# Performance work log

Measured on AMD Instinct MI355X. Metric: run time of the kernel, lower is better.

## Reference

```python
import jax, jax.numpy as jnp
import numpy as np

WIDTH = 8  # fixed-point fractional bits (init arg Width)


def quantizer(x, width=WIDTH):
    # Fixed-point quantization to `width` fractional bits, clipped to [-1, 1].
    scale = jnp.asarray(2.0 ** width, x.dtype)
    return jnp.clip(jnp.round(x * scale) / scale, -1.0, 1.0)


def setup_inputs() -> dict:
    key = jax.random.key(0)
    k1, k2, k3 = jax.random.split(key, 3)
    N, H, W, C = 32, 56, 56, 128
    KH, KW, F = 3, 3, 256
    OH, OW = H - KH + 1, W - KW + 1  # valid padding, stride 1
    x = jax.random.normal(k1, (N, H, W, C), dtype=jnp.float32) * 0.5
    kernels = jax.random.normal(k2, (KH, KW, C, F), dtype=jnp.float32) * 0.01
    bias = jax.random.normal(k3, (OH, OW, F), dtype=jnp.float32) * 0.01
    return {"x": x, "kernels": kernels, "bias": bias}


def reference(x, kernels, bias):
    # Method == 'Fixed': quantize input and kernels, valid conv, quantize output,
    # then per-position bias add + ReLU.
    xq = quantizer(x)
    wq = quantizer(kernels)
    out = jax.lax.conv_general_dilated(
        xq, wq,
        window_strides=(1, 1),
        padding="VALID",
        dimension_numbers=("NHWC", "HWIO", "NHWC"),
    )
    out = quantizer(out)
    return jax.nn.relu(out + bias[None, :, :, :])
```

## Files before the change

kernel.cpp:

```cpp
#include <hip/hip_runtime.h>
#include <hip/hip_bf16.h>
#include <stdint.h>
#include <stddef.h>


typedef float  f32x4  __attribute__((ext_vector_type(4)));
typedef short  bf16x8 __attribute__((ext_vector_type(8)));

#define N_IMG 32
#define H_IN 56
#define W_IN 56
#define C_IN 128
#define F_OUT 256
#define OHW 54
#define M_TOTAL (N_IMG * OHW * OHW)
#define BM 128
#define BN 128
#define BK 64

__device__ __forceinline__ unsigned short quant_to_bf16(float x) {
    float a = rintf(x * 256.0f);
    a = fminf(fmaxf(a, -256.0f), 256.0f);
    float q = a * 0.00390625f;
    union { float f; unsigned int u; } cv; cv.f = q;
    return (unsigned short)(cv.u >> 16);
}

__device__ __forceinline__ void async_copy16(const unsigned short* g, unsigned short* l) {
    __builtin_amdgcn_global_load_lds(
        (const __attribute__((address_space(1))) unsigned int*)g,
        (__attribute__((address_space(3))) unsigned int*)l, 16, 0, 0);
}

__global__ __launch_bounds__(256) void quant_x_kernel(
        const float* __restrict__ x, unsigned short* __restrict__ xq) {
    int i = (blockIdx.x * 256 + threadIdx.x) * 4;
    float4 v = *reinterpret_cast<const float4*>(x + i);
    ushort4 o;
    o.x = quant_to_bf16(v.x);
    o.y = quant_to_bf16(v.y);
    o.z = quant_to_bf16(v.z);
    o.w = quant_to_bf16(v.w);
    *reinterpret_cast<ushort4*>(xq + i) = o;
}

__global__ __launch_bounds__(256) void quant_w_kernel(
        const float* __restrict__ w, unsigned short* __restrict__ wp) {
    int idx = blockIdx.x * 256 + threadIdx.x;
    int c  = idx & 127;
    int f  = (idx >> 7) & 255;
    int kk = idx >> 15;
    float v = w[(kk * C_IN + c) * F_OUT + f];
    wp[idx] = quant_to_bf16(v);
}

__global__ __launch_bounds__(256) void conv_kernel(
        const unsigned short* __restrict__ xq,
        const unsigned short* __restrict__ wp,
        const float* __restrict__ bias,
        float* __restrict__ out)
{
    __shared__ __attribute__((aligned(16))) unsigned short Alds[BM * BK];
    __shared__ __attribute__((aligned(16))) unsigned short Blds[BN * BK];

    const int tid  = threadIdx.x;
    const int wave = tid >> 6;
    const int lane = tid & 63;
    const int bid  = blockIdx.x;
    const int mb   = bid >> 1;
    const int nb   = bid & 1;
    const int m0   = mb * BM;
    const int wr   = wave >> 1;
    const int wc   = wave & 1;

    const int c16  = tid & 7;
    const int row0 = tid >> 3;
    const int sw   = c16 ^ (row0 & 7);

    const unsigned short* a_base[4];
#pragma unroll
    for (int r = 0; r < 4; ++r) {
        int m = m0 + row0 + 32 * r;
        int n_img = m / (OHW * OHW);
        int rem   = m % (OHW * OHW);
        int oh = rem / OHW, ow = rem % OHW;
        a_base[r] = xq + (size_t)((n_img * H_IN + oh) * W_IN + ow) * C_IN + sw * 8;
    }
    const unsigned short* b_base[4];
#pragma unroll
    for (int r = 0; r < 4; ++r) {
        int f = nb * BN + row0 + 32 * r;
        b_base[r] = wp + (size_t)f * C_IN + sw * 8;
    }
    unsigned short* a_dst[4];
    unsigned short* b_dst[4];
#pragma unroll
    for (int r = 0; r < 4; ++r) {
        int cb = r * 256 + (tid & ~63);
        a_dst[r] = Alds + cb * 8;
        b_dst[r] = Blds + cb * 8;
    }

    const int mr = lane & 15;
    const int lq = lane >> 4;
    const int ls = lane & 7;

    f32x4 acc[4][4];
#pragma unroll
    for (int i = 0; i < 4; ++i)
#pragma unroll
        for (int j = 0; j < 4; ++j) acc[i][j] = (f32x4)(0.0f);

    for (int kk = 0; kk < 9; ++kk) {
        const int kh = kk / 3, kw = kk - 3 * kh;
        const int atap = (kh * W_IN + kw) * C_IN;
        const int btap = kk * (F_OUT * C_IN);
#pragma unroll
        for (int half = 0; half < 2; ++half) {
            const int aoff = atap + half * 64;
            const int boff = btap + half * 64;

            __syncthreads();
#pragma unroll
            for (int r = 0; r < 4; ++r)
                async_copy16(a_base[r] + aoff, a_dst[r]);
#pragma unroll
            for (int r = 0; r < 4; ++r)
                async_copy16(b_base[r] + boff, b_dst[r]);
            __syncthreads();

#pragma unroll
            for (int ks = 0; ks < 2; ++ks) {
                bf16x8 af[4], bfr[4];
#pragma unroll
                for (int mi = 0; mi < 4; ++mi)
                    af[mi] = *reinterpret_cast<const bf16x8*>(
                        Alds + (wr * 64 + mi * 16 + mr) * BK + (((ks * 4 + lq) ^ ls) * 8));
#pragma unroll
                for (int ni = 0; ni < 4; ++ni)
                    bfr[ni] = *reinterpret_cast<const bf16x8*>(
                        Blds + (wc * 64 + ni * 16 + mr) * BK + (((ks * 4 + lq) ^ ls) * 8));
#pragma unroll
                for (int mi = 0; mi < 4; ++mi)
#pragma unroll
                    for (int ni = 0; ni < 4; ++ni)
                        acc[mi][ni] = __builtin_amdgcn_mfma_f32_16x16x32_bf16(
                            af[mi], bfr[ni], acc[mi][ni], 0, 0, 0);
            }
        }
    }

    const int fcol0 = nb * BN + wc * 64 + mr;
#pragma unroll
    for (int mi = 0; mi < 4; ++mi) {
#pragma unroll
        for (int r = 0; r < 4; ++r) {
            const int m = m0 + wr * 64 + mi * 16 + lq * 4 + r;
            const float* brow = bias + (size_t)(m % (OHW * OHW)) * F_OUT;
            float* orow = out + (size_t)m * F_OUT;
#pragma unroll
            for (int ni = 0; ni < 4; ++ni) {
                float v = acc[mi][ni][r];
                float t = rintf(v * 256.0f);
                t = fminf(fmaxf(t, -256.0f), 256.0f);
                float o = t * 0.00390625f + brow[fcol0 + ni * 16];
                orow[fcol0 + ni * 16] = fmaxf(o, 0.0f);
            }
        }
    }
}

extern "C" void kernel_launch(void* const* d_in, const int* in_sizes, int n_in,
                              void* d_out, int out_size, void* d_ws, size_t ws_size,
                              hipStream_t stream) {
    (void)in_sizes; (void)n_in; (void)out_size;
    const float* x    = (const float*)d_in[0];
    const float* w    = (const float*)d_in[1];
    const float* bias = (const float*)d_in[2];
    float* out        = (float*)d_out;

    const size_t x_elems = (size_t)N_IMG * H_IN * W_IN * C_IN;
    const size_t w_elems = (size_t)9 * F_OUT * C_IN;
    const size_t xq_bytes = x_elems * sizeof(unsigned short);
    const size_t need = xq_bytes + w_elems * sizeof(unsigned short);
    if (ws_size < need) return;

    unsigned short* xq = (unsigned short*)d_ws;
    unsigned short* wp = (unsigned short*)((char*)d_ws + xq_bytes);

    quant_x_kernel<<<(int)(x_elems / (256 * 4)), 256, 0, stream>>>(x, xq);
    quant_w_kernel<<<(int)(w_elems / 256), 256, 0, stream>>>(w, wp);
    conv_kernel<<<(M_TOTAL / BM) * 2, 256, 0, stream>>>(xq, wp, bias, out);
}
```

Baseline: 92.80 us.

## Triple-buffer LDS pipeline with full-width N tile and 512-thread blocks

```diff
diff --git a/kernel.cpp b/kernel.cpp
--- a/kernel.cpp
+++ b/kernel.cpp
@@ -15,8 +15,13 @@
 #define OHW 54
 #define M_TOTAL (N_IMG * OHW * OHW)
 #define BM 128
-#define BN 128
+#define BN 256
 #define BK 64
+#define NTILES 18
+#define A_BUF_SHORTS (BM * BK)
+#define B_BUF_SHORTS (BN * BK)
+#define A_BUF_BYTES (A_BUF_SHORTS * 2)
+#define B_BUF_BYTES (B_BUF_SHORTS * 2)
 
 __device__ __forceinline__ unsigned short quant_to_bf16(float x) {
     float a = rintf(x * 256.0f);
@@ -30,6 +35,16 @@
     __builtin_amdgcn_global_load_lds(
         (const __attribute__((address_space(1))) unsigned int*)g,
         (__attribute__((address_space(3))) unsigned int*)l, 16, 0, 0);
+}
+
+__device__ __forceinline__ unsigned lds_off(const void* p) {
+    return (unsigned)(uintptr_t)(__attribute__((address_space(3))) const void*)p;
+}
+
+__device__ __forceinline__ bf16x8 lds_read_b128(unsigned addr) {
+    bf16x8 r;
+    asm volatile("ds_read_b128 %0, %1" : "=v"(r) : "v"(addr));
+    return r;
 }
 
 __global__ __launch_bounds__(256) void quant_x_kernel(
@@ -50,60 +65,65 @@
     int c  = idx & 127;
     int f  = (idx >> 7) & 255;
     int kk = idx >> 15;
-    float v = w[(kk * C_IN + c) * F_OUT + f];
-    wp[idx] = quant_to_bf16(v);
-}
-
-__global__ __launch_bounds__(256) void conv_kernel(
+    wp[idx] = quant_to_bf16(w[(kk * C_IN + c) * F_OUT + f]);
+}
+
+__global__ __launch_bounds__(512, 2) void conv_kernel(
         const unsigned short* __restrict__ xq,
         const unsigned short* __restrict__ wp,
         const float* __restrict__ bias,
         float* __restrict__ out)
 {
-    __shared__ __attribute__((aligned(16))) unsigned short Alds[BM * BK];
-    __shared__ __attribute__((aligned(16))) unsigned short Blds[BN * BK];
+    __shared__ __attribute__((aligned(16))) unsigned short Alds[3][A_BUF_SHORTS];
+    __shared__ __attribute__((aligned(16))) unsigned short Blds[3][B_BUF_SHORTS];
 
     const int tid  = threadIdx.x;
+    const int lane = tid & 63;
     const int wave = tid >> 6;
-    const int lane = tid & 63;
-    const int bid  = blockIdx.x;
-    const int mb   = bid >> 1;
-    const int nb   = bid & 1;
-    const int m0   = mb * BM;
-    const int wr   = wave >> 1;
-    const int wc   = wave & 1;
-
+    const int wr   = wave >> 2;
+    const int wc   = wave & 3;
+    const int m0   = blockIdx.x * BM;
+
+    const int rowt = tid >> 3;
     const int c16  = tid & 7;
-    const int row0 = tid >> 3;
-    const int sw   = c16 ^ (row0 & 7);
-
-    const unsigned short* a_base[4];
-#pragma unroll
-    for (int r = 0; r < 4; ++r) {
-        int m = m0 + row0 + 32 * r;
+    const int sw   = c16 ^ (rowt & 7);
+    const int dstc = tid & ~63;
+
+    const unsigned short* a_src[2];
+#pragma unroll
+    for (int r = 0; r < 2; ++r) {
+        int m = m0 + 64 * r + rowt;
         int n_img = m / (OHW * OHW);
         int rem   = m % (OHW * OHW);
         int oh = rem / OHW, ow = rem % OHW;
-        a_base[r] = xq + (size_t)((n_img * H_IN + oh) * W_IN + ow) * C_IN + sw * 8;
+        a_src[r] = xq + (size_t)((n_img * H_IN + oh) * W_IN + ow) * C_IN + sw * 8;
     }
-    const unsigned short* b_base[4];
-#pragma unroll
-    for (int r = 0; r < 4; ++r) {
-        int f = nb * BN + row0 + 32 * r;
-        b_base[r] = wp + (size_t)f * C_IN + sw * 8;
-    }
-    unsigned short* a_dst[4];
-    unsigned short* b_dst[4];
-#pragma unroll
-    for (int r = 0; r < 4; ++r) {
-        int cb = r * 256 + (tid & ~63);
-        a_dst[r] = Alds + cb * 8;
-        b_dst[r] = Blds + cb * 8;
-    }
+    const unsigned short* b_src[4];
+#pragma unroll
+    for (int r = 0; r < 4; ++r)
+        b_src[r] = wp + (size_t)(64 * r + rowt) * C_IN + sw * 8;
 
     const int mr = lane & 15;
     const int lq = lane >> 4;
-    const int ls = lane & 7;
+    unsigned a_rd[4][2], b_rd[4][2];
+    const unsigned Abase = lds_off(&Alds[0][0]);
+    const unsigned Bbase = lds_off(&Blds[0][0]);
+#pragma unroll
+    for (int mi = 0; mi < 4; ++mi)
+#pragma unroll
+        for (int ks = 0; ks < 2; ++ks) {
+            int row = wr * 64 + mi * 16 + mr;
+            int ch  = (ks * 4 + lq) ^ (mr & 7);
+            a_rd[mi][ks] = Abase + row * (BK * 2) + ch * 16;
+        }
+#pragma unroll
+    for (int ni = 0; ni < 4; ++ni)
+#pragma unroll
+        for (int ks = 0; ks < 2; ++ks) {
+            int row = wc * 64 + ni * 16 + mr;
+            int ch  = (ks * 4 + lq) ^ (mr & 7);
+            b_rd[ni][ks] = Bbase + row * (BK * 2) + ch * 16;
+        }
 
     f32x4 acc[4][4];
 #pragma unroll
@@ -111,56 +131,109 @@
 #pragma unroll
         for (int j = 0; j < 4; ++j) acc[i][j] = (f32x4)(0.0f);
 
-    for (int kk = 0; kk < 9; ++kk) {
-        const int kh = kk / 3, kw = kk - 3 * kh;
-        const int atap = (kh * W_IN + kw) * C_IN;
-        const int btap = kk * (F_OUT * C_IN);
-#pragma unroll
-        for (int half = 0; half < 2; ++half) {
-            const int aoff = atap + half * 64;
-            const int boff = btap + half * 64;
-
-            __syncthreads();
-#pragma unroll
-            for (int r = 0; r < 4; ++r)
-                async_copy16(a_base[r] + aoff, a_dst[r]);
-#pragma unroll
-            for (int r = 0; r < 4; ++r)
-                async_copy16(b_base[r] + boff, b_dst[r]);
-            __syncthreads();
-
-#pragma unroll
-            for (int ks = 0; ks < 2; ++ks) {
-                bf16x8 af[4], bfr[4];
-#pragma unroll
-                for (int mi = 0; mi < 4; ++mi)
-                    af[mi] = *reinterpret_cast<const bf16x8*>(
-                        Alds + (wr * 64 + mi * 16 + mr) * BK + (((ks * 4 + lq) ^ ls) * 8));
-#pragma unroll
-                for (int ni = 0; ni < 4; ++ni)
-                    bfr[ni] = *reinterpret_cast<const bf16x8*>(
-                        Blds + (wc * 64 + ni * 16 + mr) * BK + (((ks * 4 + lq) ^ ls) * 8));
-#pragma unroll
-                for (int mi = 0; mi < 4; ++mi)
-#pragma unroll
-                    for (int ni = 0; ni < 4; ++ni)
-                        acc[mi][ni] = __builtin_amdgcn_mfma_f32_16x16x32_bf16(
-                            af[mi], bfr[ni], acc[mi][ni], 0, 0, 0);
-            }
-        }
+    auto stage_p0 = [&](int tt, int bi) {
+        int kk = tt >> 1, half = tt & 1;
+        int kh = (kk * 43) >> 7, kw = kk - 3 * kh;
+        int aoff = (kh * W_IN + kw) * C_IN + half * 64;
+        int boff = kk * (F_OUT * C_IN) + half * 64;
+        async_copy16(a_src[0] + aoff, &Alds[bi][dstc * 8]);
+        async_copy16(a_src[1] + aoff, &Alds[bi][(512 + dstc) * 8]);
+        async_copy16(b_src[0] + boff, &Blds[bi][dstc * 8]);
+    };
+    auto stage_p1 = [&](int tt, int bi) {
+        int kk = tt >> 1, half = tt & 1;
+        int boff = kk * (F_OUT * C_IN) + half * 64;
+        async_copy16(b_src[1] + boff, &Blds[bi][(512 + dstc) * 8]);
+        async_copy16(b_src[2] + boff, &Blds[bi][(1024 + dstc) * 8]);
+        async_copy16(b_src[3] + boff, &Blds[bi][(1536 + dstc) * 8]);
+    };
+
+    auto do_tile = [&](int cur, int stage_tt, bool dostage, int endmode) {
+        const unsigned ca = (unsigned)cur * A_BUF_BYTES;
+        const unsigned cb = (unsigned)cur * B_BUF_BYTES;
+        int bi = cur + 2; if (bi >= 3) bi -= 3;
+
+        bf16x8 af[4][2], bq[2][2];
+#pragma unroll
+        for (int mi = 0; mi < 4; ++mi)
+#pragma unroll
+            for (int ks = 0; ks < 2; ++ks)
+                af[mi][ks] = lds_read_b128(a_rd[mi][ks] + ca);
+#pragma unroll
+        for (int ni = 0; ni < 2; ++ni)
+#pragma unroll
+            for (int ks = 0; ks < 2; ++ks)
+                bq[ni][ks] = lds_read_b128(b_rd[ni][ks] + cb);
+        if (dostage) stage_p0(stage_tt, bi);
+        asm volatile("" ::: "memory");
+        __builtin_amdgcn_s_barrier();
+        asm volatile("s_waitcnt lgkmcnt(0)" ::: "memory");
+        __builtin_amdgcn_sched_barrier(0);
+        __builtin_amdgcn_s_setprio(1);
+#pragma unroll
+        for (int mi = 0; mi < 4; ++mi)
+#pragma unroll
+            for (int ni = 0; ni < 2; ++ni)
+#pragma unroll
+                for (int ks = 0; ks < 2; ++ks)
+                    acc[mi][ni] = __builtin_amdgcn_mfma_f32_16x16x32_bf16(
+                        af[mi][ks], bq[ni][ks], acc[mi][ni], 0, 0, 0);
+        __builtin_amdgcn_s_setprio(0);
+        asm volatile("" ::: "memory");
+        __builtin_amdgcn_s_barrier();
+
+#pragma unroll
+        for (int ni = 0; ni < 2; ++ni)
+#pragma unroll
+            for (int ks = 0; ks < 2; ++ks)
+                bq[ni][ks] = lds_read_b128(b_rd[ni + 2][ks] + cb);
+        if (dostage) stage_p1(stage_tt, bi);
+        asm volatile("" ::: "memory");
+        __builtin_amdgcn_s_barrier();
+        asm volatile("s_waitcnt lgkmcnt(0)" ::: "memory");
+        __builtin_amdgcn_sched_barrier(0);
+        __builtin_amdgcn_s_setprio(1);
+#pragma unroll
+        for (int mi = 0; mi < 4; ++mi)
+#pragma unroll
+            for (int ni = 0; ni < 2; ++ni)
+#pragma unroll
+                for (int ks = 0; ks < 2; ++ks)
+                    acc[mi][ni + 2] = __builtin_amdgcn_mfma_f32_16x16x32_bf16(
+                        af[mi][ks], bq[ni][ks], acc[mi][ni + 2], 0, 0, 0);
+        __builtin_amdgcn_s_setprio(0);
+        if (endmode == 0)      asm volatile("s_waitcnt vmcnt(6)" ::: "memory");
+        else if (endmode == 1) asm volatile("s_waitcnt vmcnt(0)" ::: "memory");
+        if (endmode <= 1) {
+            asm volatile("" ::: "memory");
+            __builtin_amdgcn_s_barrier();
+        }
+    };
+
+    stage_p0(0, 0); stage_p1(0, 0);
+    stage_p0(1, 1); stage_p1(1, 1);
+    asm volatile("s_waitcnt vmcnt(6)" ::: "memory");
+    __builtin_amdgcn_s_barrier();
+
+#pragma unroll 1
+    for (int t = 0; t < 16; ++t) {
+        int cur = t - (t / 3) * 3;
+        do_tile(cur, t + 2, true, 0);
     }
-
-    const int fcol0 = nb * BN + wc * 64 + mr;
+    do_tile(1, 0, false, 1);
+    do_tile(2, 0, false, 2);
+
+    const int fcol0 = wc * 64 + mr;
 #pragma unroll
     for (int mi = 0; mi < 4; ++mi) {
 #pragma unroll
-        for (int r = 0; r < 4; ++r) {
-            const int m = m0 + wr * 64 + mi * 16 + lq * 4 + r;
+        for (int rr = 0; rr < 4; ++rr) {
+            const int m = m0 + wr * 64 + mi * 16 + lq * 4 + rr;
             const float* brow = bias + (size_t)(m % (OHW * OHW)) * F_OUT;
             float* orow = out + (size_t)m * F_OUT;
 #pragma unroll
             for (int ni = 0; ni < 4; ++ni) {
-                float v = acc[mi][ni][r];
+                float v = acc[mi][ni][rr];
                 float t = rintf(v * 256.0f);
                 t = fminf(fmaxf(t, -256.0f), 256.0f);
                 float o = t * 0.00390625f + brow[fcol0 + ni * 16];
@@ -190,5 +263,5 @@
 
     quant_x_kernel<<<(int)(x_elems / (256 * 4)), 256, 0, stream>>>(x, xq);
     quant_w_kernel<<<(int)(w_elems / 256), 256, 0, stream>>>(w, wp);
-    conv_kernel<<<(M_TOTAL / BM) * 2, 256, 0, stream>>>(xq, wp, bias, out);
-}
+    conv_kernel<<<M_TOTAL / BM, 512, 0, stream>>>(xq, wp, bias, out);
+}
```

New measurement: 94.98 us. 2.3% more time.

## Double-buffer LDS tiles so async global loads overlap MFMA compute

Applied to the files above, without the earlier changes.

```diff
diff --git a/kernel.cpp b/kernel.cpp
--- a/kernel.cpp
+++ b/kernel.cpp
@@ -50,18 +50,17 @@
     int c  = idx & 127;
     int f  = (idx >> 7) & 255;
     int kk = idx >> 15;
-    float v = w[(kk * C_IN + c) * F_OUT + f];
-    wp[idx] = quant_to_bf16(v);
+    wp[idx] = quant_to_bf16(w[(kk * C_IN + c) * F_OUT + f]);
 }
 
-__global__ __launch_bounds__(256) void conv_kernel(
+__global__ __launch_bounds__(256, 2) void conv_kernel(
         const unsigned short* __restrict__ xq,
         const unsigned short* __restrict__ wp,
         const float* __restrict__ bias,
         float* __restrict__ out)
 {
-    __shared__ __attribute__((aligned(16))) unsigned short Alds[BM * BK];
-    __shared__ __attribute__((aligned(16))) unsigned short Blds[BN * BK];
+    __shared__ __attribute__((aligned(16))) unsigned short Alds[2][BM * BK];
+    __shared__ __attribute__((aligned(16))) unsigned short Blds[2][BN * BK];
 
     const int tid  = threadIdx.x;
     const int wave = tid >> 6;
@@ -73,9 +72,9 @@
     const int wr   = wave >> 1;
     const int wc   = wave & 1;
 
-    const int c16  = tid & 7;
     const int row0 = tid >> 3;
-    const int sw   = c16 ^ (row0 & 7);
+    const int sw   = (tid & 7) ^ (row0 & 7);
+    const int dstc = (tid & ~63) * 8;
 
     const unsigned short* a_base[4];
 #pragma unroll
@@ -88,22 +87,24 @@
     }
     const unsigned short* b_base[4];
 #pragma unroll
-    for (int r = 0; r < 4; ++r) {
-        int f = nb * BN + row0 + 32 * r;
-        b_base[r] = wp + (size_t)f * C_IN + sw * 8;
-    }
-    unsigned short* a_dst[4];
-    unsigned short* b_dst[4];
+    for (int r = 0; r < 4; ++r)
+        b_base[r] = wp + (size_t)(nb * BN + row0 + 32 * r) * C_IN + sw * 8;
+
+    auto stage = [&](int t, unsigned short* Ab, unsigned short* Bb) {
+        int kk = t >> 1, hf = t & 1;
+        int kh = (kk * 43) >> 7, kw = kk - 3 * kh;
+        int aoff = (kh * W_IN + kw) * C_IN + hf * 64;
+        int boff = kk * (F_OUT * C_IN) + hf * 64;
 #pragma unroll
-    for (int r = 0; r < 4; ++r) {
-        int cb = r * 256 + (tid & ~63);
-        a_dst[r] = Alds + cb * 8;
-        b_dst[r] = Blds + cb * 8;
-    }
+        for (int r = 0; r < 4; ++r)
+            async_copy16(a_base[r] + aoff, Ab + r * 2048 + dstc);
+#pragma unroll
+        for (int r = 0; r < 4; ++r)
+            async_copy16(b_base[r] + boff, Bb + r * 2048 + dstc);
+    };
 
     const int mr = lane & 15;
     const int lq = lane >> 4;
-    const int ls = lane & 7;
 
     f32x4 acc[4][4];
 #pragma unroll
@@ -111,56 +112,56 @@
 #pragma unroll
         for (int j = 0; j < 4; ++j) acc[i][j] = (f32x4)(0.0f);
 
-    for (int kk = 0; kk < 9; ++kk) {
-        const int kh = kk / 3, kw = kk - 3 * kh;
-        const int atap = (kh * W_IN + kw) * C_IN;
-        const int btap = kk * (F_OUT * C_IN);
+    auto compute = [&](const unsigned short* Ab, const unsigned short* Bb) {
 #pragma unroll
-        for (int half = 0; half < 2; ++half) {
-            const int aoff = atap + half * 64;
-            const int boff = btap + half * 64;
-
-            __syncthreads();
+        for (int ks = 0; ks < 2; ++ks) {
+            const int ch = (((ks * 4 + lq) ^ (mr & 7)) * 8);
+            bf16x8 af[4], bfr[4];
 #pragma unroll
-            for (int r = 0; r < 4; ++r)
-                async_copy16(a_base[r] + aoff, a_dst[r]);
+            for (int mi = 0; mi < 4; ++mi)
+                af[mi] = *reinterpret_cast<const bf16x8*>(
+                    Ab + (wr * 64 + mi * 16 + mr) * BK + ch);
 #pragma unroll
-            for (int r = 0; r < 4; ++r)
-                async_copy16(b_base[r] + boff, b_dst[r]);
-            __syncthreads();
-
+            for (int ni = 0; ni < 4; ++ni)
+                bfr[ni] = *reinterpret_cast<const bf16x8*>(
+                    Bb + (wc * 64 + ni * 16 + mr) * BK + ch);
 #pragma unroll
-            for (int ks = 0; ks < 2; ++ks) {
-                bf16x8 af[4], bfr[4];
-#pragma unroll
-                for (int mi = 0; mi < 4; ++mi)
-                    af[mi] = *reinterpret_cast<const bf16x8*>(
-                        Alds + (wr * 64 + mi * 16 + mr) * BK + (((ks * 4 + lq) ^ ls) * 8));
+            for (int mi = 0; mi < 4; ++mi)
 #pragma unroll
                 for (int ni = 0; ni < 4; ++ni)
-                    bfr[ni] = *reinterpret_cast<const bf16x8*>(
-                        Blds + (wc * 64 + ni * 16 + mr) * BK + (((ks * 4 + lq) ^ ls) * 8));
-#pragma unroll
-                for (int mi = 0; mi < 4; ++mi)
-#pragma unroll
-                    for (int ni = 0; ni < 4; ++ni)
-                        acc[mi][ni] = __builtin_amdgcn_mfma_f32_16x16x32_bf16(
-                            af[mi], bfr[ni], acc[mi][ni], 0, 0, 0);
-            }
+                    acc[mi][ni] = __builtin_amdgcn_mfma_f32_16x16x32_bf16(
+                        af[mi], bfr[ni], acc[mi][ni], 0, 0, 0);
         }
+    };
+
+    stage(0, Alds[0], Blds[0]);
+    __syncthreads();
+
+#pragma unroll 1
+    for (int tp = 0; tp < 8; ++tp) {
+        stage(2 * tp + 1, Alds[1], Blds[1]);
+        compute(Alds[0], Blds[0]);
+        __syncthreads();
+        stage(2 * tp + 2, Alds[0], Blds[0]);
+        compute(Alds[1], Blds[1]);
+        __syncthreads();
     }
+    stage(17, Alds[1], Blds[1]);
+    compute(Alds[0], Blds[0]);
+    __syncthreads();
+    compute(Alds[1], Blds[1]);
 
     const int fcol0 = nb * BN + wc * 64 + mr;
 #pragma unroll
     for (int mi = 0; mi < 4; ++mi) {
 #pragma unroll
-        for (int r = 0; r < 4; ++r) {
-            const int m = m0 + wr * 64 + mi * 16 + lq * 4 + r;
+        for (int rr = 0; rr < 4; ++rr) {
+            const int m = m0 + wr * 64 + mi * 16 + lq * 4 + rr;
             const float* brow = bias + (size_t)(m % (OHW * OHW)) * F_OUT;
             float* orow = out + (size_t)m * F_OUT;
 #pragma unroll
             for (int ni = 0; ni < 4; ++ni) {
-                float v = acc[mi][ni][r];
+                float v = acc[mi][ni][rr];
                 float t = rintf(v * 256.0f);
                 t = fminf(fmaxf(t, -256.0f), 256.0f);
                 float o = t * 0.00390625f + brow[fcol0 + ni * 16];
```

New measurement: 96.00 us. 1.03x slower.
